# Kernel optimization log

Measured on AMD Instinct MI355X. Metric: run time of the kernel, lower is better.

## Reference

```python
import jax, jax.numpy as jnp
import numpy as np

N, E, D, H, C = 100000, 1600000, 64, 64, 16


def setup_inputs() -> dict:
    key = jax.random.key(0)
    ks = jax.random.split(key, 8)
    x = jax.random.normal(ks[0], (N, D), dtype=jnp.float32)
    edge_index = jax.random.randint(ks[1], (2, E), 0, N, dtype=jnp.int64)
    W1 = jax.random.normal(ks[2], (D, H), dtype=jnp.float32) * (1.0 / np.sqrt(D))
    b1 = jax.random.normal(ks[3], (H,), dtype=jnp.float32) * 0.01
    W2 = jax.random.normal(ks[4], (H, H), dtype=jnp.float32) * (1.0 / np.sqrt(H))
    b2 = jax.random.normal(ks[5], (H,), dtype=jnp.float32) * 0.01
    Wl = jax.random.normal(ks[6], (H, C), dtype=jnp.float32) * (1.0 / np.sqrt(H))
    bl = jax.random.normal(ks[7], (C,), dtype=jnp.float32) * 0.01
    return {"x": x, "edge_index": edge_index, "W1": W1, "b1": b1,
            "W2": W2, "b2": b2, "Wl": Wl, "bl": bl}


def reference(x, edge_index, W1, b1, W2, b2, Wl, bl):
    n = x.shape[0]
    src, dst = edge_index[0], edge_index[1]
    # GCN symmetric normalization with self-loops: deg = 1 + in-degree at dst
    deg = jax.ops.segment_sum(jnp.ones(src.shape[0], x.dtype), dst, num_segments=n) + 1.0
    inv = jax.lax.rsqrt(deg)                      # deg^{-1/2}, [N]
    norm_e = inv[src] * inv[dst]                  # per-edge norm, [E]
    self_w = inv * inv                            # self-loop weight deg^{-1}, [N]

    def gcn(h, W, b):
        h = h @ W                                 # linear transform first (PyG GCNConv)
        agg = jax.ops.segment_sum(h[src] * norm_e[:, None], dst, num_segments=n)
        agg = agg + h * self_w[:, None]           # self-loop contribution
        return agg + b

    h = jax.nn.relu(gcn(x, W1, b1))
    h = jax.nn.relu(gcn(h, W2, b2))
    return h @ Wl + bl
```

## Files before the change

kernel.cpp:

```cpp
#include <hip/hip_runtime.h>
#include <hip/hip_fp16.h>


#define WS_ALIGN 256
#define BSHIFT 8
#define MAXBUCK 512
#define CAP 6144

typedef _Float16 half8 __attribute__((ext_vector_type(8)));
typedef float floatx4 __attribute__((ext_vector_type(4)));


__global__ void k_partition(const int* __restrict__ src, const int* __restrict__ dst,
                            int* __restrict__ gcursor, int* __restrict__ spillcnt,
                            int* __restrict__ bpairs, int2* __restrict__ spill,
                            int e, int nbuck) {
    __shared__ int hist[MAXBUCK];
    __shared__ int lbase[MAXBUCK];
    const int CH = 4096;
    int base = blockIdx.x * CH;
    int end = base + CH; if (end > e) end = e;
    for (int t = threadIdx.x; t < nbuck; t += blockDim.x) hist[t] = 0;
    __syncthreads();
    for (int i = base + threadIdx.x; i < end; i += blockDim.x)
        atomicAdd(&hist[dst[i] >> BSHIFT], 1);
    __syncthreads();
    for (int t = threadIdx.x; t < nbuck; t += blockDim.x) {
        int c = hist[t];
        lbase[t] = (c > 0) ? atomicAdd(&gcursor[t], c) : 0;
        hist[t] = 0;
    }
    __syncthreads();
    for (int i = base + threadIdx.x; i < end; i += blockDim.x) {
        int s = src[i], d = dst[i];
        int b = d >> BSHIFT;
        int pos = lbase[b] + atomicAdd(&hist[b], 1);
        int packed = (s << BSHIFT) | (d & ((1 << BSHIFT) - 1));
        if (pos < CAP) bpairs[b * CAP + pos] = packed;
        else { int si = atomicAdd(spillcnt, 1); spill[si] = make_int2(b, packed); }
    }
}

__global__ void k_bscan(const int* __restrict__ gcursor, int* __restrict__ gbase,
                        int e, int nbuck) {
    __shared__ int tmp[MAXBUCK];
    int t = threadIdx.x;
    int v = (t < nbuck) ? gcursor[t] : 0;
    tmp[t] = v;
    __syncthreads();
    int x = v;
    #pragma unroll
    for (int d = 1; d < MAXBUCK; d <<= 1) {
        int y = (t >= d) ? tmp[t - d] : 0;
        __syncthreads();
        x += y;
        tmp[t] = x;
        __syncthreads();
    }
    if (t < nbuck) gbase[t] = x - v;
    if (t == 0) gbase[nbuck] = e;
}

__global__ void k_bfin(const int* __restrict__ bpairs, const int* __restrict__ gcursor,
                       const int* __restrict__ gbase, const int* __restrict__ spillcnt,
                       const int2* __restrict__ spill, int2* __restrict__ ocnt,
                       float* __restrict__ inv, int* __restrict__ ssrc, int n) {
    __shared__ int lcnt[256];
    __shared__ int tmp[256];
    __shared__ int loff[256];
    __shared__ int lcur[256];
    const int b = blockIdx.x;
    const int t = threadIdx.x;
    const int tot = gcursor[b];
    const int reg = (tot < CAP) ? tot : CAP;
    const int rb = b * CAP;
    const int lo = gbase[b];
    const int spn = *spillcnt;
    lcnt[t] = 0; lcur[t] = 0;
    __syncthreads();
    for (int i = t; i < reg; i += 256)
        atomicAdd(&lcnt[bpairs[rb + i] & 255], 1);
    for (int i = t; i < spn; i += 256) {
        int2 sp = spill[i];
        if (sp.x == b) atomicAdd(&lcnt[sp.y & 255], 1);
    }
    __syncthreads();
    int v = lcnt[t];
    tmp[t] = v;
    __syncthreads();
    int x = v;
    #pragma unroll
    for (int d = 1; d < 256; d <<= 1) {
        int y = (t >= d) ? tmp[t - d] : 0;
        __syncthreads();
        x += y;
        tmp[t] = x;
        __syncthreads();
    }
    loff[t] = x - v;
    int node = (b << BSHIFT) + t;
    if (node < n) {
        ocnt[node] = make_int2(lo + (x - v), v);
        inv[node] = rsqrtf((float)v + 1.0f);
    }
    __syncthreads();
    for (int i = t; i < reg; i += 256) {
        int p = bpairs[rb + i];
        int l = p & 255;
        int pos = lo + loff[l] + atomicAdd(&lcur[l], 1);
        ssrc[pos] = p >> BSHIFT;
    }
    for (int i = t; i < spn; i += 256) {
        int2 sp = spill[i];
        if (sp.x == b) {
            int l = sp.y & 255;
            int pos = lo + loff[l] + atomicAdd(&lcur[l], 1);
            ssrc[pos] = sp.y >> BSHIFT;
        }
    }
}


__device__ __forceinline__ void loadA(const float* in, size_t base, half8& a) {
    float4 lo = *reinterpret_cast<const float4*>(in + base);
    float4 hi = *reinterpret_cast<const float4*>(in + base + 16);
    a[0] = (_Float16)lo.x; a[1] = (_Float16)lo.y; a[2] = (_Float16)lo.z; a[3] = (_Float16)lo.w;
    a[4] = (_Float16)hi.x; a[5] = (_Float16)hi.y; a[6] = (_Float16)hi.z; a[7] = (_Float16)hi.w;
}
__device__ __forceinline__ void loadA(const __half* in, size_t base, half8& a) {
    const _Float16* p = reinterpret_cast<const _Float16*>(in + base);
    #pragma unroll
    for (int j = 0; j < 4; ++j) { a[j] = p[j]; a[4 + j] = p[16 + j]; }
}

template <typename Tin>
__global__ void __launch_bounds__(256, 4)
k_transform(const Tin* __restrict__ in, const float* __restrict__ W,
            const float* __restrict__ inv, __half* __restrict__ out, int n) {
    const int lane = threadIdx.x & 63;
    const int m = lane & 15, g = lane >> 4;
    const int wid = blockIdx.x * 4 + (threadIdx.x >> 6);
    const int nw = gridDim.x * 4;

    half8 bf[4][2];
    #pragma unroll
    for (int t = 0; t < 4; ++t)
        #pragma unroll
        for (int s = 0; s < 2; ++s) {
            #pragma unroll
            for (int j = 0; j < 4; ++j) {
                bf[t][s][j]     = (_Float16)W[(32 * s + 4 * g + j) * 64 + 16 * t + m];
                bf[t][s][4 + j] = (_Float16)W[(32 * s + 16 + 4 * g + j) * 64 + 16 * t + m];
            }
        }

    const int ntile = (n + 15) >> 4;
    for (int tile = wid; tile < ntile; tile += nw) {
        const int rbase = tile << 4;
        int arow = rbase + m; if (arow >= n) arow = n - 1;
        half8 a[2];
        loadA(in, (size_t)arow * 64 + 0  + 4 * g, a[0]);
        loadA(in, (size_t)arow * 64 + 32 + 4 * g, a[1]);

        floatx4 acc[4] = {{0.f,0.f,0.f,0.f},{0.f,0.f,0.f,0.f},{0.f,0.f,0.f,0.f},{0.f,0.f,0.f,0.f}};
        #pragma unroll
        for (int s = 0; s < 2; ++s)
            #pragma unroll
            for (int t = 0; t < 4; ++t)
                acc[t] = __builtin_amdgcn_mfma_f32_16x16x32_f16(a[s], bf[t][s], acc[t], 0, 0, 0);

        #pragma unroll
        for (int reg = 0; reg < 4; ++reg) {
            int row = rbase + 4 * g + reg;
            if (row < n) {
                float iv = inv[row];
                #pragma unroll
                for (int t = 0; t < 4; ++t)
                    out[(size_t)row * 64 + 16 * t + m] = __float2half(acc[t][reg] * iv);
            }
        }
    }
}


__global__ void __launch_bounds__(256, 8)
k_aggregate(const __half* __restrict__ t, const int* __restrict__ ssrc,
            const int2* __restrict__ ocnt, const float* __restrict__ inv,
            const float* __restrict__ b, __half* __restrict__ out,
            int n, int do_relu) {
    const int lane = threadIdx.x & 63;
    const int g = lane >> 3;
    const int f = lane & 7;
    const int wid = blockIdx.x * (blockDim.x >> 6) + (threadIdx.x >> 6);
    const int nw = gridDim.x * (blockDim.x >> 6);
    float b8[8];
    #pragma unroll
    for (int q = 0; q < 8; ++q) b8[q] = b[f * 8 + q];

    for (int node = wid; node < n; node += nw) {
        const int2 oc = ocnt[node];
        const int start = oc.x, cnt = oc.y;
        const int tot = cnt + 1;
        float acc[8] = {0.f,0.f,0.f,0.f,0.f,0.f,0.f,0.f};
        for (int be = 0; be < tot; be += 64) {
            int lim = tot - be; if (lim > 64) lim = 64;
            int myidx = (be + lane < cnt) ? ssrc[start + be + lane] : node;
            for (int j = 0; j < lim; j += 8) {
                int epos = j + g;
                int sidx = __shfl(myidx, epos);
                float wt = (epos < lim) ? 1.f : 0.f;
                float4 raw = *reinterpret_cast<const float4*>(t + (size_t)sidx * 64 + f * 8);
                const __half2* hp = reinterpret_cast<const __half2*>(&raw);
                #pragma unroll
                for (int q = 0; q < 4; ++q) {
                    float2 fv = __half22float2(hp[q]);
                    acc[2 * q]     = fmaf(fv.x, wt, acc[2 * q]);
                    acc[2 * q + 1] = fmaf(fv.y, wt, acc[2 * q + 1]);
                }
            }
        }
        #pragma unroll
        for (int off = 8; off < 64; off <<= 1)
            #pragma unroll
            for (int q = 0; q < 8; ++q)
                acc[q] += __shfl_xor(acc[q], off);
        if (g == 0) {
            const float iv = inv[node];
            __half hres[8];
            #pragma unroll
            for (int q = 0; q < 8; ++q) {
                float r = fmaf(acc[q], iv, b8[q]);
                if (do_relu) r = fmaxf(r, 0.f);
                hres[q] = __float2half(r);
            }
            *reinterpret_cast<float4*>(out + (size_t)node * 64 + f * 8) =
                *reinterpret_cast<const float4*>(hres);
        }
    }
}


__global__ void k_final(const __half* __restrict__ h, const float* __restrict__ Wl,
                        const float* __restrict__ bl, float* __restrict__ out, int n) {
    __shared__ float Ws[64 * 16];
    for (int i = threadIdx.x; i < 64 * 16; i += blockDim.x) Ws[i] = Wl[i];
    __syncthreads();
    const int lane = threadIdx.x & 63;
    const int r = lane >> 4, c = lane & 15;
    const int wid = blockIdx.x * (blockDim.x >> 6) + (threadIdx.x >> 6);
    const int nw = gridDim.x * (blockDim.x >> 6);
    const float blc = bl[c];
    for (int base = wid * 4; base < n; base += nw * 4) {
        int row = base + r;
        if (row < n) {
            float acc = blc;
            const __half* hrow = h + (size_t)row * 64;
            #pragma unroll
            for (int kk = 0; kk < 8; ++kk) {
                float4 raw = *reinterpret_cast<const float4*>(hrow + kk * 8);
                const __half2* hp = reinterpret_cast<const __half2*>(&raw);
                #pragma unroll
                for (int j = 0; j < 4; ++j) {
                    float2 fv = __half22float2(hp[j]);
                    acc = fmaf(fv.x, Ws[(kk * 8 + 2 * j + 0) * 16 + c],
                          fmaf(fv.y, Ws[(kk * 8 + 2 * j + 1) * 16 + c], acc));
                }
            }
            out[(size_t)row * 16 + c] = acc;
        }
    }
}


extern "C" void kernel_launch(void* const* d_in, const int* in_sizes, int n_in,
                              void* d_out, int out_size, void* d_ws, size_t ws_size,
                              hipStream_t stream) {
    const float* x  = (const float*)d_in[0];
    const int*   ei = (const int*)d_in[1];
    const float* W1 = (const float*)d_in[2];
    const float* b1 = (const float*)d_in[3];
    const float* W2 = (const float*)d_in[4];
    const float* b2 = (const float*)d_in[5];
    const float* Wl = (const float*)d_in[6];
    const float* bl = (const float*)d_in[7];
    float* out = (float*)d_out;

    const int n = in_sizes[0] / 64;
    const int e = in_sizes[1] / 2;
    const int* src = ei;
    const int* dst = ei + e;
    const int nbuck = (n + (1 << BSHIFT) - 1) >> BSHIFT;
    const int nchunk = (e + 4095) / 4096;

    char* ws = (char*)d_ws;
    size_t off = 0;
    auto alloc = [&](size_t bytes) -> void* {
        void* p = ws + off;
        off += (bytes + (WS_ALIGN - 1)) & ~((size_t)WS_ALIGN - 1);
        return p;
    };
    int*    gcursor = (int*)alloc((size_t)(MAXBUCK + 1) * 4);
    int*    gbase   = (int*)alloc((size_t)(MAXBUCK + 1) * 4);
    int2*   ocnt    = (int2*)alloc((size_t)n * 8);
    float*  inv     = (float*)alloc((size_t)n * 4);
    int*    ssrc    = (int*)alloc((size_t)e * 4);
    __half* bufA    = (__half*)alloc((size_t)n * 64 * 2);
    __half* bufB    = (__half*)alloc((size_t)n * 64 * 2);
    int*    bpairs  = (int*)bufA;
    int2*   spill   = (int2*)bufB;
    int*    spillcnt = gcursor + MAXBUCK;

    hipMemsetAsync(gcursor, 0, (size_t)(MAXBUCK + 1) * 4, stream);

    k_partition<<<nchunk, 256, 0, stream>>>(src, dst, gcursor, spillcnt, bpairs, spill, e, nbuck);
    k_bscan<<<1, MAXBUCK, 0, stream>>>(gcursor, gbase, e, nbuck);
    k_bfin<<<nbuck, 256, 0, stream>>>(bpairs, gcursor, gbase, spillcnt, spill, ocnt, inv, ssrc, n);

    const int ntile = (n + 15) / 16;
    const int tgrid = (ntile + 3) / 4;
    k_transform<float><<<tgrid, 256, 0, stream>>>(x, W1, inv, bufA, n);
    k_aggregate<<<2048, 256, 0, stream>>>(bufA, ssrc, ocnt, inv, b1, bufB, n, 1);
    k_transform<__half><<<tgrid, 256, 0, stream>>>(bufB, W2, inv, bufA, n);
    k_aggregate<<<2048, 256, 0, stream>>>(bufA, ssrc, ocnt, inv, b2, bufB, n, 1);
    k_final<<<2048, 256, 0, stream>>>(bufB, Wl, bl, out, n);
}
```

Baseline: 174.7 us.

## Fuse final linear into second aggregation and fold bucket scan into bfin

Removes the separate bucket prefix-scan kernel: each bfin block now sums the counts of all preceding buckets itself to find its base offset. Merges the second GCN aggregation with the output linear layer, so the 64-wide hidden activations are no longer written to and reread from global memory, and two launches are dropped. In exchange each aggregation node does a small extra per-lane dot product plus shuffle reductions, and each bfin block does a redundant partial reduction over up to about 390 counts.

```diff
diff --git a/kernel.cpp b/kernel.cpp
--- a/kernel.cpp
+++ b/kernel.cpp
@@ -41,40 +41,34 @@
     }
 }
 
-__global__ void k_bscan(const int* __restrict__ gcursor, int* __restrict__ gbase,
-                        int e, int nbuck) {
-    __shared__ int tmp[MAXBUCK];
-    int t = threadIdx.x;
-    int v = (t < nbuck) ? gcursor[t] : 0;
-    tmp[t] = v;
-    __syncthreads();
-    int x = v;
-    #pragma unroll
-    for (int d = 1; d < MAXBUCK; d <<= 1) {
-        int y = (t >= d) ? tmp[t - d] : 0;
-        __syncthreads();
-        x += y;
-        tmp[t] = x;
-        __syncthreads();
-    }
-    if (t < nbuck) gbase[t] = x - v;
-    if (t == 0) gbase[nbuck] = e;
-}
-
 __global__ void k_bfin(const int* __restrict__ bpairs, const int* __restrict__ gcursor,
-                       const int* __restrict__ gbase, const int* __restrict__ spillcnt,
-                       const int2* __restrict__ spill, int2* __restrict__ ocnt,
-                       float* __restrict__ inv, int* __restrict__ ssrc, int n) {
+                       const int* __restrict__ spillcnt, const int2* __restrict__ spill,
+                       int2* __restrict__ ocnt, float* __restrict__ inv,
+                       int* __restrict__ ssrc, int n, int nbuck) {
     __shared__ int lcnt[256];
     __shared__ int tmp[256];
     __shared__ int loff[256];
     __shared__ int lcur[256];
+    __shared__ int s_lo;
     const int b = blockIdx.x;
     const int t = threadIdx.x;
+    {
+        int partial = 0;
+        for (int i = t; i < b; i += 256) partial += gcursor[i];
+        tmp[t] = partial;
+        __syncthreads();
+        #pragma unroll
+        for (int d = 128; d > 0; d >>= 1) {
+            if (t < d) tmp[t] += tmp[t + d];
+            __syncthreads();
+        }
+        if (t == 0) s_lo = tmp[0];
+        __syncthreads();
+    }
+    const int lo = s_lo;
     const int tot = gcursor[b];
     const int reg = (tot < CAP) ? tot : CAP;
     const int rb = b * CAP;
-    const int lo = gbase[b];
     const int spn = *spillcnt;
     lcnt[t] = 0; lcur[t] = 0;
     __syncthreads();
@@ -240,33 +234,65 @@
 }
 
 
-__global__ void k_final(const __half* __restrict__ h, const float* __restrict__ Wl,
-                        const float* __restrict__ bl, float* __restrict__ out, int n) {
-    __shared__ float Ws[64 * 16];
-    for (int i = threadIdx.x; i < 64 * 16; i += blockDim.x) Ws[i] = Wl[i];
-    __syncthreads();
+__global__ void __launch_bounds__(256, 8)
+k_aggfin(const __half* __restrict__ t, const int* __restrict__ ssrc,
+         const int2* __restrict__ ocnt, const float* __restrict__ inv,
+         const float* __restrict__ b, const float* __restrict__ Wl,
+         const float* __restrict__ bl, float* __restrict__ out, int n) {
     const int lane = threadIdx.x & 63;
-    const int r = lane >> 4, c = lane & 15;
+    const int g = lane >> 3;
+    const int f = lane & 7;
     const int wid = blockIdx.x * (blockDim.x >> 6) + (threadIdx.x >> 6);
     const int nw = gridDim.x * (blockDim.x >> 6);
-    const float blc = bl[c];
-    for (int base = wid * 4; base < n; base += nw * 4) {
-        int row = base + r;
-        if (row < n) {
-            float acc = blc;
-            const __half* hrow = h + (size_t)row * 64;
-            #pragma unroll
-            for (int kk = 0; kk < 8; ++kk) {
-                float4 raw = *reinterpret_cast<const float4*>(hrow + kk * 8);
+    float b8[8], wl0[8], wl1[8];
+    #pragma unroll
+    for (int q = 0; q < 8; ++q) {
+        b8[q] = b[f * 8 + q];
+        wl0[q] = Wl[(f * 8 + q) * 16 + 2 * g];
+        wl1[q] = Wl[(f * 8 + q) * 16 + 2 * g + 1];
+    }
+    const float bl0 = bl[2 * g], bl1 = bl[2 * g + 1];
+
+    for (int node = wid; node < n; node += nw) {
+        const int2 oc = ocnt[node];
+        const int start = oc.x, cnt = oc.y;
+        const int tot = cnt + 1;
+        float acc[8] = {0.f,0.f,0.f,0.f,0.f,0.f,0.f,0.f};
+        for (int be = 0; be < tot; be += 64) {
+            int lim = tot - be; if (lim > 64) lim = 64;
+            int myidx = (be + lane < cnt) ? ssrc[start + be + lane] : node;
+            for (int j = 0; j < lim; j += 8) {
+                int epos = j + g;
+                int sidx = __shfl(myidx, epos);
+                float wt = (epos < lim) ? 1.f : 0.f;
+                float4 raw = *reinterpret_cast<const float4*>(t + (size_t)sidx * 64 + f * 8);
                 const __half2* hp = reinterpret_cast<const __half2*>(&raw);
                 #pragma unroll
-                for (int j = 0; j < 4; ++j) {
-                    float2 fv = __half22float2(hp[j]);
-                    acc = fmaf(fv.x, Ws[(kk * 8 + 2 * j + 0) * 16 + c],
-                          fmaf(fv.y, Ws[(kk * 8 + 2 * j + 1) * 16 + c], acc));
+                for (int q = 0; q < 4; ++q) {
+                    float2 fv = __half22float2(hp[q]);
+                    acc[2 * q]     = fmaf(fv.x, wt, acc[2 * q]);
+                    acc[2 * q + 1] = fmaf(fv.y, wt, acc[2 * q + 1]);
                 }
             }
-            out[(size_t)row * 16 + c] = acc;
+        }
+        #pragma unroll
+        for (int off = 8; off < 64; off <<= 1)
+            #pragma unroll
+            for (int q = 0; q < 8; ++q)
+                acc[q] += __shfl_xor(acc[q], off);
+        const float iv = inv[node];
+        float p0 = 0.f, p1 = 0.f;
+        #pragma unroll
+        for (int q = 0; q < 8; ++q) {
+            float h = fmaxf(fmaf(acc[q], iv, b8[q]), 0.f);
+            p0 = fmaf(h, wl0[q], p0);
+            p1 = fmaf(h, wl1[q], p1);
+        }
+        p0 += __shfl_xor(p0, 1); p0 += __shfl_xor(p0, 2); p0 += __shfl_xor(p0, 4);
+        p1 += __shfl_xor(p1, 1); p1 += __shfl_xor(p1, 2); p1 += __shfl_xor(p1, 4);
+        if (f == 0) {
+            float2 o = make_float2(p0 + bl0, p1 + bl1);
+            *reinterpret_cast<float2*>(out + (size_t)node * 16 + 2 * g) = o;
         }
     }
 }
@@ -300,7 +326,6 @@
         return p;
     };
     int*    gcursor = (int*)alloc((size_t)(MAXBUCK + 1) * 4);
-    int*    gbase   = (int*)alloc((size_t)(MAXBUCK + 1) * 4);
     int2*   ocnt    = (int2*)alloc((size_t)n * 8);
     float*  inv     = (float*)alloc((size_t)n * 4);
     int*    ssrc    = (int*)alloc((size_t)e * 4);
@@ -313,14 +338,12 @@
     hipMemsetAsync(gcursor, 0, (size_t)(MAXBUCK + 1) * 4, stream);
 
     k_partition<<<nchunk, 256, 0, stream>>>(src, dst, gcursor, spillcnt, bpairs, spill, e, nbuck);
-    k_bscan<<<1, MAXBUCK, 0, stream>>>(gcursor, gbase, e, nbuck);
-    k_bfin<<<nbuck, 256, 0, stream>>>(bpairs, gcursor, gbase, spillcnt, spill, ocnt, inv, ssrc, n);
+    k_bfin<<<nbuck, 256, 0, stream>>>(bpairs, gcursor, spillcnt, spill, ocnt, inv, ssrc, n, nbuck);
 
     const int ntile = (n + 15) / 16;
     const int tgrid = (ntile + 3) / 4;
     k_transform<float><<<tgrid, 256, 0, stream>>>(x, W1, inv, bufA, n);
     k_aggregate<<<2048, 256, 0, stream>>>(bufA, ssrc, ocnt, inv, b1, bufB, n, 1);
     k_transform<__half><<<tgrid, 256, 0, stream>>>(bufB, W2, inv, bufA, n);
-    k_aggregate<<<2048, 256, 0, stream>>>(bufA, ssrc, ocnt, inv, b2, bufB, n, 1);
-    k_final<<<2048, 256, 0, stream>>>(bufB, Wl, bl, out, n);
-}
+    k_aggfin<<<2048, 256, 0, stream>>>(bufA, ssrc, ocnt, inv, b2, Wl, bl, out, n);
+}
```

After: 176.8 us. About the same (+1.2%).
